# Performance work log

Hardware: AMD Instinct MI355X
Metric: run time of the kernel (lower is better)

Reference implementation:

```python
import math
import jax, jax.numpy as jnp
import numpy as np

D, DK, DV = 256, 256, 256

def setup_inputs() -> dict:
    key = jax.random.key(0)
    ks = jax.random.split(key, 7)
    s = 1.0 / math.sqrt(D)
    return {
        "x": jax.random.normal(ks[0], (4, 4096, D), dtype=jnp.float32),
        "Wq": jax.random.uniform(ks[1], (D, DK), jnp.float32, -s, s),
        "bq": jax.random.uniform(ks[2], (DK,), jnp.float32, -s, s),
        "Wk": jax.random.uniform(ks[3], (D, DK), jnp.float32, -s, s),
        "bk": jax.random.uniform(ks[4], (DK,), jnp.float32, -s, s),
        "Wv": jax.random.uniform(ks[5], (D, DV), jnp.float32, -s, s),
        "bv": jax.random.uniform(ks[6], (DV,), jnp.float32, -s, s),
    }

def reference(x, Wq, bq, Wk, bk, Wv, bv):
    # x: [B, S, D]
    q = x @ Wq + bq            # [B, S, DK]
    k = x @ Wk + bk            # [B, S, DK]
    v = x @ Wv + bv            # [B, S, DV]
    scores = jnp.einsum('bqd,bkd->bqk', q, k) / math.sqrt(DK)  # [B, S, S]
    S = x.shape[1]
    causal = jnp.tril(jnp.ones((S, S), dtype=bool))  # True = keep
    scores = jnp.where(causal, scores, -jnp.inf)
    attn = jax.nn.softmax(scores, axis=-1)
    return jnp.einsum('bqk,bkd->bqd', attn, v)  # [B, S, DV]
```

## Files before the change

kernel.cpp:

```cpp
#include <hip/hip_runtime.h>
#include <cmath>

#define LOG2E 1.4426950408889634f

typedef __attribute__((ext_vector_type(8))) __bf16 bf16x8;
typedef __attribute__((ext_vector_type(4))) float f32x4;
typedef __attribute__((ext_vector_type(16))) float f32x16;
typedef __attribute__((ext_vector_type(4))) float float4v;
typedef __attribute__((ext_vector_type(8))) unsigned short ushort8;
typedef __attribute__((ext_vector_type(4))) unsigned int uint4v;
typedef __attribute__((ext_vector_type(2))) int int2v;

__device__ __forceinline__ unsigned short f2bf(float f) {
  unsigned int u = __builtin_bit_cast(unsigned int, f);
  u += 0x7fffu + ((u >> 16) & 1u);
  return (unsigned short)(u >> 16);
}

__device__ __forceinline__ unsigned int cvtpk(float lo, float hi) {
  unsigned int r;
  asm volatile("v_cvt_pk_bf16_f32 %0, %1, %2" : "=v"(r) : "v"(lo), "v"(hi));
  return r;
}

__device__ __forceinline__ void gload_lds16(const unsigned short* g, unsigned short* l) {
  __builtin_amdgcn_global_load_lds(
      (const __attribute__((address_space(1))) unsigned int*)(const void*)g,
      (__attribute__((address_space(3))) unsigned int*)(void*)l, 16, 0, 0);
}

__global__ __launch_bounds__(256) void prep_w_kernel(
    const float* __restrict__ Wq, const float* __restrict__ Wk,
    const float* __restrict__ Wv, unsigned short* __restrict__ Wt) {
  const int w = blockIdx.y, n = blockIdx.x, k = threadIdx.x;
  const float* W = (w == 0) ? Wq : ((w == 1) ? Wk : Wv);
  const float s = (w == 0) ? (LOG2E / 16.0f) : 1.0f;
  Wt[w * 65536 + n * 256 + k] = f2bf(W[k * 256 + n] * s);
}

__global__ __launch_bounds__(256) void proj_kernel(
    const float* __restrict__ x, const unsigned short* __restrict__ Wt,
    const float* __restrict__ bq, const float* __restrict__ bk,
    const float* __restrict__ bv,
    unsigned short* __restrict__ q_o, unsigned short* __restrict__ k_o,
    unsigned short* __restrict__ vt_o) {
  const int mt = blockIdx.x;
  const int nfh = blockIdx.y;
  const int tid = threadIdx.x;
  const int wid = tid >> 6, lane = tid & 63, g = (lane >> 4) & 3, c = lane & 15;
  const int row_base = mt * 64 + wid * 16;

  bf16x8 a[8];
  const float* xr = x + (size_t)(row_base + c) * 256;
#pragma unroll
  for (int s = 0; s < 8; ++s) {
    const float4v v0 = *(const float4v*)(xr + s * 32 + g * 8);
    const float4v v1 = *(const float4v*)(xr + s * 32 + g * 8 + 4);
    union { bf16x8 v; unsigned short u[8]; } t;
#pragma unroll
    for (int j = 0; j < 4; ++j) { t.u[j] = f2bf(v0[j]); t.u[4 + j] = f2bf(v1[j]); }
    a[s] = t.v;
  }

  for (int w = 0; w < 3; ++w) {
    const float* bias = (w == 0) ? bq : ((w == 1) ? bk : bv);
    const float bscale = (w == 0) ? (LOG2E / 16.0f) : 1.0f;
    const unsigned short* wtb = Wt + w * 65536;
#pragma unroll
    for (int nfi = 0; nfi < 8; ++nfi) {
      const int nf = nfh * 8 + nfi;
      f32x4 acc = (f32x4){0.f, 0.f, 0.f, 0.f};
      const unsigned short* wr = wtb + (size_t)(nf * 16 + c) * 256;
#pragma unroll
      for (int s = 0; s < 8; ++s) {
        bf16x8 b = *(const bf16x8*)(wr + s * 32 + g * 8);
        acc = __builtin_amdgcn_mfma_f32_16x16x32_bf16(a[s], b, acc, 0, 0, 0);
      }
      const float bvl = bias[nf * 16 + c] * bscale;
#pragma unroll
      for (int r = 0; r < 4; ++r) {
        const int row = row_base + g * 4 + r;
        const unsigned short ov = f2bf(acc[r] + bvl);
        if (w == 0) {
          q_o[(size_t)row * 256 + nf * 16 + c] = ov;
        } else if (w == 1) {
          k_o[(size_t)row * 256 + nf * 16 + c] = ov;
        } else {
          const int b_ = row >> 12, s_ = row & 4095;
          vt_o[((size_t)b_ * 256 + nf * 16 + c) * 4096 + s_] = ov;
        }
      }
    }
  }
}

__global__ __launch_bounds__(256, 1) void attn_kernel(
    const unsigned short* __restrict__ qg, const unsigned short* __restrict__ kg,
    const unsigned short* __restrict__ vtg, float* __restrict__ out) {
  __shared__ unsigned short Klds[2][64 * 256];
  __shared__ unsigned short Vlds[2][256 * 64];
  __shared__ float llds[2][2][32];

  const int tid = threadIdx.x;
  const int wid = tid >> 6, lane = tid & 63;
  const int hi = lane >> 5, q5 = lane & 31;
  const int tl = wid >> 1, wk = wid & 1;
  const int bid = blockIdx.x;
  const int b = bid >> 6, j = bid & 63;
  const int T = j + 1;

  const unsigned short* qb = qg + (size_t)b * 4096 * 256;
  const unsigned short* kb = kg + (size_t)b * 4096 * 256;
  const unsigned short* vb = vtg + (size_t)b * 256 * 4096;
  float* outb = out + (size_t)b * 4096 * 256;

  const int q0 = j * 64 + tl * 32;
  const int qrow = q0 + q5;

  int koff[8], voff[8];
#pragma unroll
  for (int i = 0; i < 8; ++i) {
    const int kr = wid * 16 + i * 2 + (lane >> 5);
    const int c8 = (lane & 31) ^ (kr & 7);
    koff[i] = kr * 256 + c8 * 8;
    const int d = wid * 64 + i * 8 + (lane >> 3);
    const int c8v = (lane & 7) ^ (d & 7);
    voff[i] = d * 4096 + c8v * 8;
  }

  auto stage = [&](int bufn, int t) {
    const unsigned short* kp = kb + t * (64 * 256);
    const unsigned short* vp = vb + t * 64;
#pragma unroll
    for (int i = 0; i < 8; ++i)
      gload_lds16(kp + koff[i], &Klds[bufn][(wid * 8 + i) * 512]);
#pragma unroll
    for (int i = 0; i < 8; ++i)
      gload_lds16(vp + voff[i], &Vlds[bufn][(wid * 8 + i) * 512]);
  };

  bf16x8 bqf[16];
  {
    const unsigned short* qr = qb + (size_t)qrow * 256;
#pragma unroll
    for (int s = 0; s < 16; ++s) bqf[s] = *(const bf16x8*)(qr + s * 16 + hi * 8);
  }

  float l = 0.f;
  f32x16 o[8];
#pragma unroll
  for (int d = 0; d < 8; ++d)
#pragma unroll
    for (int r = 0; r < 16; ++r) o[d][r] = 0.f;

  const int krow = wk * 32 + q5;
  const int ksw = (krow & 7) << 3;
  const int kbase = krow * 256;

  int kcolr[16];
#pragma unroll
  for (int r = 0; r < 16; ++r) kcolr[r] = wk * 32 + (r & 3) + 8 * (r >> 2) + 4 * hi;

  stage(0, 0);
  for (int t = 0; t < T; ++t) {
    const int bufn = t & 1;
    __syncthreads();
    if (t + 1 < T) stage(bufn ^ 1, t + 1);

    f32x16 sa, sb;
#pragma unroll
    for (int r = 0; r < 16; ++r) { sa[r] = 0.f; sb[r] = 0.f; }
#pragma unroll
    for (int s = 0; s < 8; ++s) {
      bf16x8 ka0 = *(const bf16x8*)(&Klds[bufn][(kbase + s * 16 + hi * 8) ^ ksw]);
      bf16x8 ka1 = *(const bf16x8*)(&Klds[bufn][(kbase + (s + 8) * 16 + hi * 8) ^ ksw]);
      sa = __builtin_amdgcn_mfma_f32_32x32x16_bf16(ka0, bqf[s], sa, 0, 0, 0);
      sb = __builtin_amdgcn_mfma_f32_32x32x16_bf16(ka1, bqf[s + 8], sb, 0, 0, 0);
    }
    f32x16 sc = sa + sb;

    if (t == j) {
#pragma unroll
      for (int r = 0; r < 16; ++r)
        if (t * 64 + kcolr[r] > qrow) sc[r] = -1e30f;
    }

    float p[16];
#pragma unroll
    for (int r = 0; r < 16; ++r) p[r] = __builtin_amdgcn_exp2f(sc[r]);
    {
      float s0 = (p[0] + p[1]) + (p[2] + p[3]);
      float s1 = (p[4] + p[5]) + (p[6] + p[7]);
      float s2 = (p[8] + p[9]) + (p[10] + p[11]);
      float s3 = (p[12] + p[13]) + (p[14] + p[15]);
      l += (s0 + s1) + (s2 + s3);
    }

    bf16x8 pfrag[2];
#pragma unroll
    for (int s2 = 0; s2 < 2; ++s2) {
      const int base = s2 * 8;
      unsigned int X = cvtpk(p[base + 0], p[base + 1]);
      unsigned int Y = cvtpk(p[base + 2], p[base + 3]);
      unsigned int Z = cvtpk(p[base + 4], p[base + 5]);
      unsigned int W = cvtpk(p[base + 6], p[base + 7]);
#if __has_builtin(__builtin_amdgcn_permlane32_swap)
      int2v rx = __builtin_amdgcn_permlane32_swap((int)X, (int)Z, false, false);
      int2v ry = __builtin_amdgcn_permlane32_swap((int)Y, (int)W, false, false);
      uint4v u = (uint4v){(unsigned)rx[0], (unsigned)ry[0], (unsigned)rx[1], (unsigned)ry[1]};
#else
      const unsigned int Xp = __shfl_xor((int)X, 32);
      const unsigned int Yp = __shfl_xor((int)Y, 32);
      const unsigned int Zp = __shfl_xor((int)Z, 32);
      const unsigned int Wp = __shfl_xor((int)W, 32);
      uint4v u = (uint4v){hi ? Zp : X, hi ? Wp : Y, hi ? Z : Xp, hi ? W : Yp};
#endif
      pfrag[s2] = __builtin_bit_cast(bf16x8, u);
    }

#pragma unroll
    for (int dblk = 0; dblk < 8; ++dblk) {
      const int drow = dblk * 32 + q5;
      const int vsw = (drow & 7) << 3;
      const int vbase = drow * 64 + wk * 32;
#pragma unroll
      for (int s2 = 0; s2 < 2; ++s2) {
        bf16x8 va = *(const bf16x8*)(&Vlds[bufn][(vbase + s2 * 16 + hi * 8) ^ vsw]);
        o[dblk] = __builtin_amdgcn_mfma_f32_32x32x16_bf16(va, pfrag[s2], o[dblk], 0, 0, 0);
      }
    }
  }

  l += __shfl_xor(l, 32);
  if (hi == 0 && lane < 32) llds[tl][wk][q5] = l;
  __syncthreads();
  const float L = l + llds[tl][wk ^ 1][q5];
  const float scale = 1.0f / L;

  float* Oex = (float*)Klds;
  float* oz = Oex + tl * (256 * 32);
  if (wk == 1) {
#pragma unroll
    for (int dblk = 0; dblk < 8; ++dblk)
#pragma unroll
      for (int r = 0; r < 16; ++r) {
        const int d = dblk * 32 + (r & 3) + 8 * (r >> 2) + 4 * hi;
        oz[d * 32 + q5] = o[dblk][r] * scale;
      }
  }
  __syncthreads();
  if (wk == 0) {
#pragma unroll
    for (int dblk = 0; dblk < 8; ++dblk) {
#pragma unroll
      for (int q2 = 0; q2 < 4; ++q2) {
        float4v val;
#pragma unroll
        for (int e = 0; e < 4; ++e) {
          const int r = q2 * 4 + e;
          const int d = dblk * 32 + e + 8 * q2 + 4 * hi;
          val[e] = o[dblk][r] * scale + oz[d * 32 + q5];
        }
        *(float4v*)(outb + (size_t)qrow * 256 + dblk * 32 + 8 * q2 + 4 * hi) = val;
      }
    }
  }
}

extern "C" void kernel_launch(void* const* d_in, const int* in_sizes, int n_in,
                              void* d_out, int out_size, void* d_ws, size_t ws_size,
                              hipStream_t stream) {
  (void)in_sizes; (void)n_in; (void)out_size; (void)ws_size;
  const float* x  = (const float*)d_in[0];
  const float* Wq = (const float*)d_in[1];
  const float* bq = (const float*)d_in[2];
  const float* Wk = (const float*)d_in[3];
  const float* bk = (const float*)d_in[4];
  const float* Wv = (const float*)d_in[5];
  const float* bv = (const float*)d_in[6];
  float* out = (float*)d_out;

  unsigned short* qs  = (unsigned short*)d_ws;
  unsigned short* ks  = qs  + (size_t)16384 * 256;
  unsigned short* vts = ks  + (size_t)16384 * 256;
  unsigned short* Wt  = vts + (size_t)16384 * 256;

  prep_w_kernel<<<dim3(256, 3), 256, 0, stream>>>(Wq, Wk, Wv, Wt);
  proj_kernel<<<dim3(256, 2), 256, 0, stream>>>(x, Wt, bq, bk, bv, qs, ks, vts);
  attn_kernel<<<256, 256, 0, stream>>>(qs, ks, vts, out);
}
```

Before: 192.9 us.

## Split attention work across d-halves, single-buffer LDS for two blocks per CU, fuse QKV projection

The attention kernel now gives each block a 32-row query tile and splits the V output dimension across wave pairs, halving the accumulator registers. It drops the LDS double buffer so two blocks can fit per CU, and launches 512 blocks ordered longest-first to balance the causal load. The projection kernel computes Q, K and V together in one pass over all 16 column fragments, removing the second grid dimension. Loading the next tile now waits behind an extra barrier instead of overlapping with compute, and each block repeats the QK^T product for its query tile, which adds redundant score work.

```diff
diff --git a/kernel.cpp b/kernel.cpp
--- a/kernel.cpp
+++ b/kernel.cpp
@@ -45,7 +45,6 @@
     unsigned short* __restrict__ q_o, unsigned short* __restrict__ k_o,
     unsigned short* __restrict__ vt_o) {
   const int mt = blockIdx.x;
-  const int nfh = blockIdx.y;
   const int tid = threadIdx.x;
   const int wid = tid >> 6, lane = tid & 63, g = (lane >> 4) & 3, c = lane & 15;
   const int row_base = mt * 64 + wid * 16;
@@ -62,59 +61,63 @@
     a[s] = t.v;
   }
 
-  for (int w = 0; w < 3; ++w) {
-    const float* bias = (w == 0) ? bq : ((w == 1) ? bk : bv);
-    const float bscale = (w == 0) ? (LOG2E / 16.0f) : 1.0f;
-    const unsigned short* wtb = Wt + w * 65536;
-#pragma unroll
-    for (int nfi = 0; nfi < 8; ++nfi) {
-      const int nf = nfh * 8 + nfi;
-      f32x4 acc = (f32x4){0.f, 0.f, 0.f, 0.f};
-      const unsigned short* wr = wtb + (size_t)(nf * 16 + c) * 256;
-#pragma unroll
-      for (int s = 0; s < 8; ++s) {
-        bf16x8 b = *(const bf16x8*)(wr + s * 32 + g * 8);
-        acc = __builtin_amdgcn_mfma_f32_16x16x32_bf16(a[s], b, acc, 0, 0, 0);
-      }
-      const float bvl = bias[nf * 16 + c] * bscale;
-#pragma unroll
-      for (int r = 0; r < 4; ++r) {
-        const int row = row_base + g * 4 + r;
-        const unsigned short ov = f2bf(acc[r] + bvl);
-        if (w == 0) {
-          q_o[(size_t)row * 256 + nf * 16 + c] = ov;
-        } else if (w == 1) {
-          k_o[(size_t)row * 256 + nf * 16 + c] = ov;
-        } else {
-          const int b_ = row >> 12, s_ = row & 4095;
-          vt_o[((size_t)b_ * 256 + nf * 16 + c) * 4096 + s_] = ov;
-        }
-      }
-    }
-  }
-}
-
-__global__ __launch_bounds__(256, 1) void attn_kernel(
+  const unsigned short* w0 = Wt;
+  const unsigned short* w1 = Wt + 65536;
+  const unsigned short* w2 = Wt + 131072;
+
+#pragma unroll
+  for (int nf = 0; nf < 16; ++nf) {
+    f32x4 aq = (f32x4){0.f, 0.f, 0.f, 0.f};
+    f32x4 ak = (f32x4){0.f, 0.f, 0.f, 0.f};
+    f32x4 av = (f32x4){0.f, 0.f, 0.f, 0.f};
+    const unsigned short* r0 = w0 + (size_t)(nf * 16 + c) * 256;
+    const unsigned short* r1 = w1 + (size_t)(nf * 16 + c) * 256;
+    const unsigned short* r2 = w2 + (size_t)(nf * 16 + c) * 256;
+#pragma unroll
+    for (int s = 0; s < 8; ++s) {
+      bf16x8 b0 = *(const bf16x8*)(r0 + s * 32 + g * 8);
+      bf16x8 b1 = *(const bf16x8*)(r1 + s * 32 + g * 8);
+      bf16x8 b2 = *(const bf16x8*)(r2 + s * 32 + g * 8);
+      aq = __builtin_amdgcn_mfma_f32_16x16x32_bf16(a[s], b0, aq, 0, 0, 0);
+      ak = __builtin_amdgcn_mfma_f32_16x16x32_bf16(a[s], b1, ak, 0, 0, 0);
+      av = __builtin_amdgcn_mfma_f32_16x16x32_bf16(a[s], b2, av, 0, 0, 0);
+    }
+    const float bql = bq[nf * 16 + c] * (LOG2E / 16.0f);
+    const float bkl = bk[nf * 16 + c];
+    const float bvl = bv[nf * 16 + c];
+#pragma unroll
+    for (int r = 0; r < 4; ++r) {
+      const int row = row_base + g * 4 + r;
+      q_o[(size_t)row * 256 + nf * 16 + c] = f2bf(aq[r] + bql);
+      k_o[(size_t)row * 256 + nf * 16 + c] = f2bf(ak[r] + bkl);
+      const int b_ = row >> 12, s_ = row & 4095;
+      vt_o[((size_t)b_ * 256 + nf * 16 + c) * 4096 + s_] = f2bf(av[r] + bvl);
+    }
+  }
+}
+
+__global__ __launch_bounds__(256, 2) void attn_kernel(
     const unsigned short* __restrict__ qg, const unsigned short* __restrict__ kg,
     const unsigned short* __restrict__ vtg, float* __restrict__ out) {
-  __shared__ unsigned short Klds[2][64 * 256];
-  __shared__ unsigned short Vlds[2][256 * 64];
-  __shared__ float llds[2][2][32];
+  __shared__ unsigned short Klds[64 * 256];
+  __shared__ unsigned short Vlds[256 * 64];
+  __shared__ float llds[2][32];
 
   const int tid = threadIdx.x;
   const int wid = tid >> 6, lane = tid & 63;
   const int hi = lane >> 5, q5 = lane & 31;
-  const int tl = wid >> 1, wk = wid & 1;
+  const int wk = wid & 1, dh = wid >> 1;
   const int bid = blockIdx.x;
-  const int b = bid >> 6, j = bid & 63;
-  const int T = j + 1;
+  const int half = bid >> 8, k6 = (bid >> 2) & 63, b = bid & 3;
+  const int qt = half ? k6 : 127 - k6;
+  const int T = (qt >> 1) + 1;
 
   const unsigned short* qb = qg + (size_t)b * 4096 * 256;
   const unsigned short* kb = kg + (size_t)b * 4096 * 256;
   const unsigned short* vb = vtg + (size_t)b * 256 * 4096;
   float* outb = out + (size_t)b * 4096 * 256;
 
-  const int q0 = j * 64 + tl * 32;
+  const int q0 = qt * 32;
   const int qrow = q0 + q5;
 
   int koff[8], voff[8];
@@ -128,15 +131,15 @@
     voff[i] = d * 4096 + c8v * 8;
   }
 
-  auto stage = [&](int bufn, int t) {
+  auto stage = [&](int t) {
     const unsigned short* kp = kb + t * (64 * 256);
     const unsigned short* vp = vb + t * 64;
 #pragma unroll
     for (int i = 0; i < 8; ++i)
-      gload_lds16(kp + koff[i], &Klds[bufn][(wid * 8 + i) * 512]);
+      gload_lds16(kp + koff[i], &Klds[(wid * 8 + i) * 512]);
 #pragma unroll
     for (int i = 0; i < 8; ++i)
-      gload_lds16(vp + voff[i], &Vlds[bufn][(wid * 8 + i) * 512]);
+      gload_lds16(vp + voff[i], &Vlds[(wid * 8 + i) * 512]);
   };
 
   bf16x8 bqf[16];
@@ -147,9 +150,9 @@
   }
 
   float l = 0.f;
-  f32x16 o[8];
-#pragma unroll
-  for (int d = 0; d < 8; ++d)
+  f32x16 o[4];
+#pragma unroll
+  for (int d = 0; d < 4; ++d)
 #pragma unroll
     for (int r = 0; r < 16; ++r) o[d][r] = 0.f;
 
@@ -161,25 +164,23 @@
 #pragma unroll
   for (int r = 0; r < 16; ++r) kcolr[r] = wk * 32 + (r & 3) + 8 * (r >> 2) + 4 * hi;
 
-  stage(0, 0);
+  stage(0);
   for (int t = 0; t < T; ++t) {
-    const int bufn = t & 1;
     __syncthreads();
-    if (t + 1 < T) stage(bufn ^ 1, t + 1);
 
     f32x16 sa, sb;
 #pragma unroll
     for (int r = 0; r < 16; ++r) { sa[r] = 0.f; sb[r] = 0.f; }
 #pragma unroll
     for (int s = 0; s < 8; ++s) {
-      bf16x8 ka0 = *(const bf16x8*)(&Klds[bufn][(kbase + s * 16 + hi * 8) ^ ksw]);
-      bf16x8 ka1 = *(const bf16x8*)(&Klds[bufn][(kbase + (s + 8) * 16 + hi * 8) ^ ksw]);
+      bf16x8 ka0 = *(const bf16x8*)(&Klds[(kbase + s * 16 + hi * 8) ^ ksw]);
+      bf16x8 ka1 = *(const bf16x8*)(&Klds[(kbase + (s + 8) * 16 + hi * 8) ^ ksw]);
       sa = __builtin_amdgcn_mfma_f32_32x32x16_bf16(ka0, bqf[s], sa, 0, 0, 0);
       sb = __builtin_amdgcn_mfma_f32_32x32x16_bf16(ka1, bqf[s + 8], sb, 0, 0, 0);
     }
     f32x16 sc = sa + sb;
 
-    if (t == j) {
+    if (t == T - 1) {
 #pragma unroll
       for (int r = 0; r < 16; ++r)
         if (t * 64 + kcolr[r] > qrow) sc[r] = -1e30f;
@@ -219,49 +220,53 @@
     }
 
 #pragma unroll
-    for (int dblk = 0; dblk < 8; ++dblk) {
-      const int drow = dblk * 32 + q5;
+    for (int dblk = 0; dblk < 4; ++dblk) {
+      const int drow = (dh * 4 + dblk) * 32 + q5;
       const int vsw = (drow & 7) << 3;
       const int vbase = drow * 64 + wk * 32;
 #pragma unroll
       for (int s2 = 0; s2 < 2; ++s2) {
-        bf16x8 va = *(const bf16x8*)(&Vlds[bufn][(vbase + s2 * 16 + hi * 8) ^ vsw]);
+        bf16x8 va = *(const bf16x8*)(&Vlds[(vbase + s2 * 16 + hi * 8) ^ vsw]);
         o[dblk] = __builtin_amdgcn_mfma_f32_32x32x16_bf16(va, pfrag[s2], o[dblk], 0, 0, 0);
       }
     }
+
+    if (t + 1 < T) {
+      __syncthreads();
+      stage(t + 1);
+    }
   }
 
   l += __shfl_xor(l, 32);
-  if (hi == 0 && lane < 32) llds[tl][wk][q5] = l;
+  if (dh == 0 && hi == 0) llds[wk][q5] = l;
   __syncthreads();
-  const float L = l + llds[tl][wk ^ 1][q5];
+  const float L = llds[0][q5] + llds[1][q5];
   const float scale = 1.0f / L;
 
-  float* Oex = (float*)Klds;
-  float* oz = Oex + tl * (256 * 32);
+  float* oz = (float*)Klds;
   if (wk == 1) {
 #pragma unroll
-    for (int dblk = 0; dblk < 8; ++dblk)
+    for (int dblk = 0; dblk < 4; ++dblk)
 #pragma unroll
       for (int r = 0; r < 16; ++r) {
-        const int d = dblk * 32 + (r & 3) + 8 * (r >> 2) + 4 * hi;
-        oz[d * 32 + q5] = o[dblk][r] * scale;
+        const int dg = (dh * 4 + dblk) * 32 + (r & 3) + 8 * (r >> 2) + 4 * hi;
+        oz[dg * 32 + q5] = o[dblk][r];
       }
   }
   __syncthreads();
   if (wk == 0) {
 #pragma unroll
-    for (int dblk = 0; dblk < 8; ++dblk) {
+    for (int dblk = 0; dblk < 4; ++dblk) {
 #pragma unroll
       for (int q2 = 0; q2 < 4; ++q2) {
         float4v val;
 #pragma unroll
         for (int e = 0; e < 4; ++e) {
           const int r = q2 * 4 + e;
-          const int d = dblk * 32 + e + 8 * q2 + 4 * hi;
-          val[e] = o[dblk][r] * scale + oz[d * 32 + q5];
+          const int dg = (dh * 4 + dblk) * 32 + e + 8 * q2 + 4 * hi;
+          val[e] = (o[dblk][r] + oz[dg * 32 + q5]) * scale;
         }
-        *(float4v*)(outb + (size_t)qrow * 256 + dblk * 32 + 8 * q2 + 4 * hi) = val;
+        *(float4v*)(outb + (size_t)qrow * 256 + (dh * 4 + dblk) * 32 + 8 * q2 + 4 * hi) = val;
       }
     }
   }
@@ -286,6 +291,6 @@
   unsigned short* Wt  = vts + (size_t)16384 * 256;
 
   prep_w_kernel<<<dim3(256, 3), 256, 0, stream>>>(Wq, Wk, Wv, Wt);
-  proj_kernel<<<dim3(256, 2), 256, 0, stream>>>(x, Wt, bq, bk, bv, qs, ks, vts);
-  attn_kernel<<<256, 256, 0, stream>>>(qs, ks, vts, out);
-}
+  proj_kernel<<<256, 256, 0, stream>>>(x, Wt, bq, bk, bv, qs, ks, vts);
+  attn_kernel<<<512, 256, 0, stream>>>(qs, ks, vts, out);
+}
```

Result: faster. 173.1 us (-10.3%).
